# Optimization experiments

Measured on AMD Instinct MI355X. Metric: run time of the kernel, lower is better.

Reference implementation:

```python
import jax, jax.numpy as jnp
import numpy as np

B, D, S, K, A = 4096, 256, 32, 8192, 256
BETA = 0.25  # vq_commitment_beta


def _ln(x, g, b):
    m = jnp.mean(x, axis=-1, keepdims=True)
    v = jnp.var(x, axis=-1, keepdims=True)
    return (x - m) * jax.lax.rsqrt(v + 1e-5) * g + b


def _clin(zr, zi, Wr, Wi, br, bi):
    # torch ComplexLinear: real = Wr(zr) - Wi(zi); imag = Wi(zr) + Wr(zi)
    return (zr @ Wr.T + br) - (zi @ Wi.T + bi), (zr @ Wi.T + bi) + (zi @ Wr.T + br)


def _forward(x_t_r, x_t_i, gw_r, gw_i, mem_r, mem_i, input_gate, vq_emb,
             vis_pal, aud_pal, mem_gate_W, mem_gate_b, mem_addr_W, mem_addr_b,
             mn_gr, mn_br, mn_gi, mn_bi,
             gq_Wr, gq_Wi, gq_br, gq_bi, gk_Wr, gk_Wi, gk_br, gk_bi,
             gv_Wr, gv_Wi, gv_br, gv_bi, sp_Wr, sp_Wi, sp_br, sp_bi,
             cr_Wr, cr_Wi, cr_br, cr_bi):
    # input gate blend (forward_step preamble)
    alpha = jax.nn.sigmoid(input_gate)
    gr = alpha * gw_r + (1.0 - alpha) * x_t_r
    gi = alpha * gw_i + (1.0 - alpha) * x_t_i
    z_flat = jnp.concatenate([gr, gi], -1)  # [B, 2D]

    # ---- EMA_VQ (eval path): cdist + argmin + straight-through ----
    d2 = (jnp.sum(z_flat ** 2, 1, keepdims=True) + jnp.sum(vq_emb ** 2, 1)
          - 2.0 * (z_flat @ vq_emb.T))  # [B, K]
    idx = jnp.argmin(d2, -1)
    z_q = vq_emb[idx]
    vq_loss = BETA * jnp.mean((jax.lax.stop_gradient(z_q) - z_flat) ** 2, -1)
    v_out = z_flat + jax.lax.stop_gradient(z_q - z_flat)
    probs = jnp.mean(jax.nn.one_hot(idx, K, dtype=jnp.float32), 0)
    batch_ent = -jnp.sum(probs * jnp.log(probs + 1e-10)) / jnp.log(jnp.asarray(K, jnp.float32))

    # ---- HermitianGating ----
    qr, qi = _clin(gr, gi, gq_Wr, gq_Wi, gq_br, gq_bi)
    kr, ki = _clin(gr, gi, gk_Wr, gk_Wi, gk_br, gk_bi)
    vr, vi = _clin(gr, gi, gv_Wr, gv_Wi, gv_br, gv_bi)
    gate = jax.nn.sigmoid(jnp.sum(qr * kr + qi * ki, -1, keepdims=True))  # Re(q k*)
    g_out = jnp.concatenate([vr * gate, vi * gate], -1)

    # ---- AssociativeMemory: content read + gated soft-scatter write ----
    sim = jnp.einsum('bsd,bd->bs', mem_r, gr) + jnp.einsum('bsd,bd->bs', mem_i, gi)  # Re(mem* q)
    attn = jax.nn.softmax(sim, -1)
    read_r = jnp.einsum('bs,bsd->bd', attn, mem_r)
    read_i = jnp.einsum('bs,bsd->bd', attn, mem_i)
    m_out = jnp.concatenate([read_r, read_i], -1)
    wgate = jax.nn.sigmoid(z_flat @ mem_gate_W.T + mem_gate_b)  # [B,1]
    ww = jax.nn.softmax(z_flat @ mem_addr_W.T + mem_addr_b, -1)  # [B,S]
    slot_ent = jnp.mean(-jnp.sum(ww * jnp.log(ww + 1e-10), -1))
    eff = wgate[:, :, None] * ww[:, :, None]  # [B,S,1]
    nm_r = _ln((1.0 - eff) * mem_r + eff * gr[:, None, :], mn_gr, mn_br)
    nm_i = _ln((1.0 - eff) * mem_i + eff * gi[:, None, :], mn_gi, mn_bi)

    # ---- HebbianSensory palette attention ----
    sr, si = _clin(gr, gi, sp_Wr, sp_Wi, sp_br, sp_bi)
    zf2 = jnp.concatenate([sr, si], -1)
    vis_attn = jax.nn.softmax(zf2 @ vis_pal.T, -1)
    aud_attn = jax.nn.softmax(zf2 @ aud_pal.T, -1)
    vis = vis_attn @ vis_pal
    aud = aud_attn @ aud_pal
    # experience = vis_c + i*aud_c
    s_out = jnp.concatenate([vis[:, :D] - aud[:, D:], vis[:, D:] + aud[:, :D]], -1)

    # ---- Critic: i * ComplexLinear(z) ----
    c_r, c_i = _clin(gr, gi, cr_Wr, cr_Wi, cr_br, cr_bi)
    c_out = jnp.concatenate([-c_i, c_r], -1)

    out_main = jnp.stack([v_out, g_out, m_out, s_out, c_out], 1)  # [B,5,2D]
    return out_main, nm_r, nm_i, idx, vq_loss, batch_ent, slot_ent


def setup_inputs():
    key = jax.random.key(0)
    ks = iter(jax.random.split(key, 48))
    n = lambda shape, s=1.0: jax.random.normal(next(ks), shape, dtype=jnp.float32) * s
    inp = {
        'x_t_r': n((B, D)), 'x_t_i': n((B, D)),
        'gw_r': n((B, D)), 'gw_i': n((B, D)),
        'mem_r': n((B, S, D)), 'mem_i': n((B, S, D)),
        'input_gate': jnp.zeros((), jnp.float32),
        'vq_emb': jax.random.uniform(next(ks), (K, 2 * D), jnp.float32, -1.0 / np.sqrt(D), 1.0 / np.sqrt(D)),
        'vis_pal': n((A, 2 * D)), 'aud_pal': n((A, 2 * D)),
        'mem_gate_W': n((1, 2 * D), 0.02), 'mem_gate_b': jnp.zeros((1,), jnp.float32),
        'mem_addr_W': n((S, 2 * D), 0.02), 'mem_addr_b': jnp.zeros((S,), jnp.float32),
        'mn_gr': jnp.ones((D,), jnp.float32), 'mn_br': jnp.zeros((D,), jnp.float32),
        'mn_gi': jnp.ones((D,), jnp.float32), 'mn_bi': jnp.zeros((D,), jnp.float32),
    }
    for p in ('gq', 'gk', 'gv', 'sp', 'cr'):
        inp[p + '_Wr'] = n((D, D), 0.05)
        inp[p + '_Wi'] = n((D, D), 0.05)
        inp[p + '_br'] = jnp.zeros((D,), jnp.float32)
        inp[p + '_bi'] = jnp.zeros((D,), jnp.float32)
    return inp


def reference(x_t_r, x_t_i, gw_r, gw_i, mem_r, mem_i, input_gate, vq_emb,
              vis_pal, aud_pal, mem_gate_W, mem_gate_b, mem_addr_W, mem_addr_b,
              mn_gr, mn_br, mn_gi, mn_bi,
              gq_Wr, gq_Wi, gq_br, gq_bi, gk_Wr, gk_Wi, gk_br, gk_bi,
              gv_Wr, gv_Wi, gv_br, gv_bi, sp_Wr, sp_Wi, sp_br, sp_bi,
              cr_Wr, cr_Wi, cr_br, cr_bi):
    return _forward(x_t_r, x_t_i, gw_r, gw_i, mem_r, mem_i, input_gate, vq_emb,
                    vis_pal, aud_pal, mem_gate_W, mem_gate_b, mem_addr_W, mem_addr_b,
                    mn_gr, mn_br, mn_gi, mn_bi,
                    gq_Wr, gq_Wi, gq_br, gq_bi, gk_Wr, gk_Wi, gk_br, gk_bi,
                    gv_Wr, gv_Wi, gv_br, gv_bi, sp_Wr, sp_Wi, sp_br, sp_bi,
                    cr_Wr, cr_Wi, cr_br, cr_bi)
```

## Files before the change

kernel.cpp:

```cpp
#include <hip/hip_runtime.h>
#include <hip/hip_bf16.h>
#include <math.h>

#define BN 4096
#define DN 256
#define SN 32
#define KN 8192
#define AN 256
#define TWO_D 512

typedef unsigned short ushort;
using bf16x8 = __attribute__((ext_vector_type(8))) short;
using f32x4  = __attribute__((ext_vector_type(4))) float;

#define OUT_MAIN 0ull
#define OUT_NMR  10485760ull
#define OUT_NMI  44040192ull
#define OUT_IDX  77594624ull
#define OUT_VQL  77598720ull
#define OUT_BENT 77602816ull
#define OUT_SENT 77602817ull

#define MBYTE (1024ull*1024ull)
#define WS_GR    (0ull)
#define WS_GI    (4ull*MBYTE)
#define WS_Z2H   (8ull*MBYTE)
#define WS_Z2L   (12ull*MBYTE)
#define WS_EH    (16ull*MBYTE)
#define WS_EL    (24ull*MBYTE)
#define WS_E2    (32ull*MBYTE)
#define WS_WBIG  (33ull*MBYTE)
#define WS_BIAS  (36ull*MBYTE)
#define WS_PALC  (37ull*MBYTE)
#define WS_VIST  (38ull*MBYTE)
#define WS_AUDT  (39ull*MBYTE)
#define WS_PVAL  (40ull*MBYTE)
#define WS_PIDX  (42ull*MBYTE)
#define WS_HIST  (44ull*MBYTE)
#define WS_SENT  (44ull*MBYTE + 64ull*1024ull)
#define WS_CL    (45ull*MBYTE)
#define WS_LOGIT (65ull*MBYTE)
#define WS_ATTN  (73ull*MBYTE)
#define WS_VIS   (77ull*MBYTE)
#define WS_AUD   (85ull*MBYTE)

#define DEVINL __device__ __forceinline__

DEVINL ushort f2bf(float f) {
    union { float f; unsigned u; } v; v.f = f;
    unsigned r = v.u + 0x7fffu + ((v.u >> 16) & 1u);
    return (ushort)(r >> 16);
}
DEVINL float bf2f(ushort h) {
    union { unsigned u; float f; } v; v.u = ((unsigned)h) << 16;
    return v.f;
}
DEVINL float sigmoidf_(float x) { return 1.f / (1.f + __expf(-x)); }

__global__ __launch_bounds__(256) void k_prep_vq(const float* __restrict__ emb,
                                                 ushort* __restrict__ eh,
                                                 ushort* __restrict__ el,
                                                 float* __restrict__ e2) {
    int t = threadIdx.x, w = t >> 6, lane = t & 63;
    int row = blockIdx.x * 4 + w;
    const float* er = emb + (size_t)row * 512;
    float acc = 0.f;
    #pragma unroll
    for (int j = 0; j < 8; j++) {
        int k = lane + 64 * j;
        float e = er[k];
        ushort h = f2bf(e);
        eh[(size_t)row * 512 + k] = h;
        el[(size_t)row * 512 + k] = f2bf(e - bf2f(h));
        acc += e * e;
    }
    for (int m = 1; m < 64; m <<= 1) acc += __shfl_xor(acc, m, 64);
    if (lane == 0) e2[row] = acc;
}

__global__ void k_prep_wbig(const float* __restrict__ Wr, const float* __restrict__ Wi,
                            const float* __restrict__ br, const float* __restrict__ bi,
                            ushort* __restrict__ Wb, float* __restrict__ bias) {
    int idx = blockIdx.x * 256 + threadIdx.x;
    int j = idx >> 9, k = idx & 511;
    int part = j >> 8, jj = j & 255;
    float v;
    if (part == 0) v = (k < 256) ? Wr[jj * 256 + k] : -Wi[jj * 256 + (k - 256)];
    else           v = (k < 256) ? Wi[jj * 256 + k] :  Wr[jj * 256 + (k - 256)];
    Wb[idx] = f2bf(v);
    if (k == 0) bias[j] = part ? (br[jj] + bi[jj]) : (br[jj] - bi[jj]);
}

__global__ void k_prep_palcat(const float* __restrict__ vis, const float* __restrict__ aud,
                              ushort* __restrict__ palc) {
    int idx = blockIdx.x * 256 + threadIdx.x;
    int a = idx >> 9, k = idx & 511;
    float v = (a < 256) ? vis[a * 512 + k] : aud[(a - 256) * 512 + k];
    palc[idx] = f2bf(v);
}
__global__ void k_prep_palT(const float* __restrict__ vis, const float* __restrict__ aud,
                            ushort* __restrict__ visT, ushort* __restrict__ audT) {
    int idx = blockIdx.x * 256 + threadIdx.x;
    int j = idx >> 8, a = idx & 255;
    visT[j * 256 + a] = f2bf(vis[a * 512 + j]);
    audT[j * 256 + a] = f2bf(aud[a * 512 + j]);
}

__global__ void k_gate(const float* __restrict__ xr, const float* __restrict__ xi,
                       const float* __restrict__ gwr, const float* __restrict__ gwi,
                       const float* __restrict__ ig,
                       float* __restrict__ gr, float* __restrict__ gi,
                       ushort* __restrict__ z2h, ushort* __restrict__ z2l) {
    int i = blockIdx.x * 256 + threadIdx.x;
    float a = sigmoidf_(ig[0]);
    float r  = a * gwr[i] + (1.f - a) * xr[i];
    float im = a * gwi[i] + (1.f - a) * xi[i];
    gr[i] = r; gi[i] = im;
    int b = i >> 8, d = i & 255;
    size_t z = (size_t)b * 512;
    ushort rh = f2bf(r);  z2h[z + d] = rh;       z2l[z + d] = f2bf(r - bf2f(rh));
    ushort ih = f2bf(im); z2h[z + 256 + d] = ih; z2l[z + 256 + d] = f2bf(im - bf2f(ih));
}

__global__ __launch_bounds__(256) void k_vq_gemm(
    const ushort* __restrict__ Zh, const ushort* __restrict__ Zl,
    const ushort* __restrict__ Eh, const ushort* __restrict__ El,
    const float* __restrict__ e2, float* __restrict__ pval, int* __restrict__ pidx) {
    __shared__ ushort Ah[128 * 40], Al[128 * 40], Bh[128 * 40], Bl[128 * 40];
    const int m0 = blockIdx.y * 128, n0 = blockIdx.x * 128;
    const int t = threadIdx.x;
    const int w = t >> 6, lane = t & 63, q = lane >> 4, ln = lane & 15;
    const int wm = w >> 1, wn = w & 1;
    f32x4 acc[4][4] = {};
    const int lrow = t >> 2, lcol = (t & 3) * 8;
    for (int k0 = 0; k0 < 512; k0 += 32) {
        __syncthreads();
        #pragma unroll
        for (int rep = 0; rep < 2; rep++) {
            int r = lrow + rep * 64;
            *(uint4*)(&Ah[r * 40 + lcol]) = *(const uint4*)(Zh + (size_t)(m0 + r) * 512 + k0 + lcol);
            *(uint4*)(&Al[r * 40 + lcol]) = *(const uint4*)(Zl + (size_t)(m0 + r) * 512 + k0 + lcol);
            *(uint4*)(&Bh[r * 40 + lcol]) = *(const uint4*)(Eh + (size_t)(n0 + r) * 512 + k0 + lcol);
            *(uint4*)(&Bl[r * 40 + lcol]) = *(const uint4*)(El + (size_t)(n0 + r) * 512 + k0 + lcol);
        }
        __syncthreads();
        bf16x8 ah[4], al[4], bh[4], bl[4];
        #pragma unroll
        for (int i = 0; i < 4; i++) {
            int ar = wm * 64 + i * 16 + ln;
            ah[i] = *(const bf16x8*)(&Ah[ar * 40 + q * 8]);
            al[i] = *(const bf16x8*)(&Al[ar * 40 + q * 8]);
            int br = wn * 64 + i * 16 + ln;
            bh[i] = *(const bf16x8*)(&Bh[br * 40 + q * 8]);
            bl[i] = *(const bf16x8*)(&Bl[br * 40 + q * 8]);
        }
        #pragma unroll
        for (int i = 0; i < 4; i++)
            #pragma unroll
            for (int j = 0; j < 4; j++) {
                acc[i][j] = __builtin_amdgcn_mfma_f32_16x16x32_bf16(ah[i], bh[j], acc[i][j], 0, 0, 0);
                acc[i][j] = __builtin_amdgcn_mfma_f32_16x16x32_bf16(ah[i], bl[j], acc[i][j], 0, 0, 0);
                acc[i][j] = __builtin_amdgcn_mfma_f32_16x16x32_bf16(al[i], bh[j], acc[i][j], 0, 0, 0);
            }
    }
    float e2v[4]; int cidx[4];
    #pragma unroll
    for (int j = 0; j < 4; j++) { cidx[j] = n0 + wn * 64 + j * 16 + ln; e2v[j] = e2[cidx[j]]; }
    #pragma unroll
    for (int i = 0; i < 4; i++) {
        #pragma unroll
        for (int reg = 0; reg < 4; reg++) {
            float bv = 3.4e38f; int bc = 0x7fffffff;
            #pragma unroll
            for (int j = 0; j < 4; j++) {
                float s = e2v[j] - 2.f * acc[i][j][reg];
                if (s < bv || (s == bv && cidx[j] < bc)) { bv = s; bc = cidx[j]; }
            }
            for (int m = 1; m < 16; m <<= 1) {
                float ov = __shfl_xor(bv, m, 64);
                int   oc = __shfl_xor(bc, m, 64);
                if (ov < bv || (ov == bv && oc < bc)) { bv = ov; bc = oc; }
            }
            if (ln == 0) {
                int r = m0 + wm * 64 + i * 16 + q * 4 + reg;
                int slot = blockIdx.x * 2 + wn;
                pval[(size_t)r * 128 + slot] = bv;
                pidx[(size_t)r * 128 + slot] = bc;
            }
        }
    }
}

__global__ __launch_bounds__(256) void k_vqfin(
    const float* __restrict__ pval, const int* __restrict__ pidx,
    const float* __restrict__ emb, const float* __restrict__ gr,
    const float* __restrict__ gi, float* __restrict__ out, int* __restrict__ hist) {
    __shared__ float sz[512];
    __shared__ float sv[128];
    __shared__ int   scd[128];
    __shared__ int   topc[8];
    __shared__ double tsc[8];
    __shared__ int   sbc;
    int b = blockIdx.x, t = threadIdx.x;
    sz[t]       = gr[(size_t)b * 256 + t];
    sz[256 + t] = gi[(size_t)b * 256 + t];
    if (t < 128) { sv[t] = pval[(size_t)b * 128 + t]; scd[t] = pidx[(size_t)b * 128 + t]; }
    __syncthreads();
    if (t == 0) {
        for (int j = 0; j < 8; j++) {
            float bv = 3.4e38f; int bi = 0;
            for (int m = 0; m < 128; m++) {
                float v = sv[m];
                if (v < bv || (v == bv && scd[m] < scd[bi])) { bv = v; bi = m; }
            }
            topc[j] = scd[bi];
            sv[bi] = 3.4e38f;
        }
    }
    __syncthreads();
    int w = t >> 6, lane = t & 63;
    for (int rep = 0; rep < 2; rep++) {
        int j = w + rep * 4;
        int c = topc[j];
        const float* e = emb + (size_t)c * 512;
        double acc = 0.0;
        #pragma unroll
        for (int u = 0; u < 8; u++) {
            int k2 = lane + u * 64;
            double d = (double)sz[k2] - (double)e[k2];
            acc += d * d;
        }
        for (int m = 1; m < 64; m <<= 1) acc += __shfl_xor(acc, m, 64);
        if (lane == 0) tsc[j] = acc;
    }
    __syncthreads();
    if (t == 0) {
        double bv = tsc[0]; int bc = topc[0];
        for (int j = 1; j < 8; j++)
            if (tsc[j] < bv || (tsc[j] == bv && topc[j] < bc)) { bv = tsc[j]; bc = topc[j]; }
        sbc = bc;
        out[OUT_IDX + b] = (float)bc;
        out[OUT_VQL + b] = (float)(0.25 * bv / 512.0);
        atomicAdd(&hist[bc], 1);
    }
    __syncthreads();
    const float* e = emb + (size_t)sbc * 512;
    float* om = out + (size_t)b * 2560;
    om[t]       = e[t];
    om[256 + t] = e[256 + t];
}

__global__ __launch_bounds__(256) void k_gemm(
    const ushort* __restrict__ A, int lda,
    const ushort* __restrict__ Bm, int ldb,
    void* __restrict__ C, int ldc,
    int Kd, const float* __restrict__ bias, int obf) {
    __shared__ ushort As[128 * 40], Bs[128 * 40];
    const int m0 = blockIdx.y * 128, n0 = blockIdx.x * 128;
    const int t = threadIdx.x;
    const int w = t >> 6, lane = t & 63, q = lane >> 4, ln = lane & 15;
    const int wm = w >> 1, wn = w & 1;
    f32x4 acc[4][4] = {};
    const int lrow = t >> 2, lcol = (t & 3) * 8;
    for (int k0 = 0; k0 < Kd; k0 += 32) {
        __syncthreads();
        #pragma unroll
        for (int rep = 0; rep < 2; rep++) {
            int r = lrow + rep * 64;
            *(uint4*)(&As[r * 40 + lcol]) = *(const uint4*)(A + (size_t)(m0 + r) * lda + k0 + lcol);
            *(uint4*)(&Bs[r * 40 + lcol]) = *(const uint4*)(Bm + (size_t)(n0 + r) * ldb + k0 + lcol);
        }
        __syncthreads();
        bf16x8 af[4], bfr[4];
        #pragma unroll
        for (int i = 0; i < 4; i++) {
            af[i]  = *(const bf16x8*)(&As[(wm * 64 + i * 16 + ln) * 40 + q * 8]);
            bfr[i] = *(const bf16x8*)(&Bs[(wn * 64 + i * 16 + ln) * 40 + q * 8]);
        }
        #pragma unroll
        for (int i = 0; i < 4; i++)
            #pragma unroll
            for (int j = 0; j < 4; j++)
                acc[i][j] = __builtin_amdgcn_mfma_f32_16x16x32_bf16(af[i], bfr[j], acc[i][j], 0, 0, 0);
    }
    #pragma unroll
    for (int i = 0; i < 4; i++) {
        int r = m0 + wm * 64 + i * 16 + q * 4;
        #pragma unroll
        for (int j = 0; j < 4; j++) {
            int c = n0 + wn * 64 + j * 16 + ln;
            float bb = bias ? bias[c] : 0.f;
            #pragma unroll
            for (int reg = 0; reg < 4; reg++) {
                float v = acc[i][j][reg] + bb;
                if (obf) ((ushort*)C)[(size_t)(r + reg) * ldc + c] = f2bf(v);
                else     ((float*)C)[(size_t)(r + reg) * ldc + c] = v;
            }
        }
    }
}

__global__ __launch_bounds__(256) void k_hermit(const ushort* __restrict__ CL,
                                                float* __restrict__ out) {
    int b = blockIdx.x, t = threadIdx.x;
    const ushort* row = CL + (size_t)b * 2560;
    float qr = bf2f(row[t]), qi = bf2f(row[256 + t]);
    float kr = bf2f(row[512 + t]), ki = bf2f(row[768 + t]);
    float part = qr * kr + qi * ki;
    __shared__ float red[4];
    for (int m = 1; m < 64; m <<= 1) part += __shfl_xor(part, m, 64);
    if ((t & 63) == 0) red[t >> 6] = part;
    __syncthreads();
    float gate = sigmoidf_(red[0] + red[1] + red[2] + red[3]);
    float vr = bf2f(row[1024 + t]), vi = bf2f(row[1280 + t]);
    float* om = out + (size_t)b * 2560;
    om[512 + t] = vr * gate; om[512 + 256 + t] = vi * gate;
    float crr = bf2f(row[2048 + t]), cii = bf2f(row[2304 + t]);
    om[4 * 512 + t] = -cii; om[4 * 512 + 256 + t] = crr;
}

__global__ __launch_bounds__(256) void k_smax(const float* __restrict__ L,
                                              ushort* __restrict__ attn) {
    int b = blockIdx.x, t = threadIdx.x;
    __shared__ float sred[8];
    for (int h = 0; h < 2; h++) {
        float x = L[(size_t)b * 512 + h * 256 + t];
        float mx = x;
        for (int m = 1; m < 64; m <<= 1) mx = fmaxf(mx, __shfl_xor(mx, m, 64));
        if ((t & 63) == 0) sred[t >> 6] = mx;
        __syncthreads();
        mx = fmaxf(fmaxf(sred[0], sred[1]), fmaxf(sred[2], sred[3]));
        float e = __expf(x - mx);
        float su = e;
        for (int m = 1; m < 64; m <<= 1) su += __shfl_xor(su, m, 64);
        if ((t & 63) == 0) sred[4 + (t >> 6)] = su;
        __syncthreads();
        su = sred[4] + sred[5] + sred[6] + sred[7];
        attn[(size_t)b * 512 + h * 256 + t] = f2bf(e / su);
        __syncthreads();
    }
}

__global__ void k_sout(const float* __restrict__ vis, const float* __restrict__ aud,
                       float* __restrict__ out) {
    int i = blockIdx.x * 256 + threadIdx.x;
    int b = i >> 8, d = i & 255;
    const float* v = vis + (size_t)b * 512;
    const float* a = aud + (size_t)b * 512;
    float* om = out + (size_t)b * 2560 + 3 * 512;
    om[d]       = v[d] - a[256 + d];
    om[256 + d] = v[256 + d] + a[d];
}

__global__ __launch_bounds__(256) void k_mem(
    const float* __restrict__ mem_r, const float* __restrict__ mem_i,
    const float* __restrict__ gr, const float* __restrict__ gi,
    const float* __restrict__ gateW, const float* __restrict__ gateB,
    const float* __restrict__ addrW, const float* __restrict__ addrB,
    const float* __restrict__ mgr, const float* __restrict__ mbr,
    const float* __restrict__ mgi, const float* __restrict__ mbi,
    float* __restrict__ out, float* __restrict__ sent) {
    __shared__ float sg[512];
    __shared__ float prt[256], prt2[256];
    __shared__ float ssim[32], swwl[32], satt[32], seff[32];
    __shared__ float smn[32], srs[32];
    int b = blockIdx.x, t = threadIdx.x;
    const float* mr = mem_r + (size_t)b * 8192;
    const float* mi = mem_i + (size_t)b * 8192;
    sg[t]       = gr[(size_t)b * 256 + t];
    sg[256 + t] = gi[(size_t)b * 256 + t];
    __syncthreads();

    {
        int s = t >> 3, j0 = (t & 7) * 32;
        float p = 0.f;
        for (int d = j0; d < j0 + 32; d++)
            p += mr[s * 256 + d] * sg[d] + mi[s * 256 + d] * sg[256 + d];
        prt[t] = p;
    }
    __syncthreads();
    if (t < 32) {
        float v = 0.f;
        for (int j = 0; j < 8; j++) v += prt[t * 8 + j];
        ssim[t] = v;
    }
    __syncthreads();
    {
        int s = t >> 3, j0 = (t & 7) * 64;
        const float* Wrow = addrW + s * 512;
        float p = 0.f;
        for (int k = j0; k < j0 + 64; k++) p += sg[k] * Wrow[k];
        prt[t] = p;
    }
    __syncthreads();
    if (t < 32) {
        float v = addrB[t];
        for (int j = 0; j < 8; j++) v += prt[t * 8 + j];
        swwl[t] = v;
    }
    __syncthreads();
    prt[t] = sg[t] * gateW[t] + sg[256 + t] * gateW[256 + t];
    __syncthreads();
    if (t == 0) {
        float acc = gateB[0];
        for (int j = 0; j < 256; j++) acc += prt[j];
        float wg = sigmoidf_(acc);
        float mx = ssim[0];
        for (int s = 1; s < 32; s++) mx = fmaxf(mx, ssim[s]);
        float su = 0.f;
        for (int s = 0; s < 32; s++) su += __expf(ssim[s] - mx);
        for (int s = 0; s < 32; s++) satt[s] = __expf(ssim[s] - mx) / su;
        mx = swwl[0];
        for (int s = 1; s < 32; s++) mx = fmaxf(mx, swwl[s]);
        su = 0.f;
        for (int s = 0; s < 32; s++) su += __expf(swwl[s] - mx);
        float ent = 0.f;
        for (int s = 0; s < 32; s++) {
            float wv = __expf(swwl[s] - mx) / su;
            ent += -wv * __logf(wv + 1e-10f);
            seff[s] = wg * wv;
        }
        atomicAdd(sent, ent * (1.f / 4096.f));
    }
    __syncthreads();
    {
        float rr = 0.f, ri = 0.f;
        for (int s = 0; s < 32; s++) {
            float a = satt[s];
            rr += a * mr[s * 256 + t];
            ri += a * mi[s * 256 + t];
        }
        float* om = out + (size_t)b * 2560 + 1024;
        om[t] = rr; om[256 + t] = ri;
    }
    for (int half = 0; half < 2; half++) {
        const float* mm  = half ? mi  : mr;
        const float* gg  = half ? mgi : mgr;
        const float* bb2 = half ? mbi : mbr;
        size_t base = (half ? OUT_NMI : OUT_NMR) + (size_t)b * 8192;
        __syncthreads();
        {
            int s = t >> 3, j0 = (t & 7) * 32;
            float eff = seff[s];
            float su = 0.f, sq = 0.f;
            for (int d = j0; d < j0 + 32; d++) {
                float x = (1.f - eff) * mm[s * 256 + d] + eff * sg[half * 256 + d];
                su += x; sq += x * x;
            }
            prt[t] = su; prt2[t] = sq;
        }
        __syncthreads();
        if (t < 32) {
            float su = 0.f, sq = 0.f;
            for (int j = 0; j < 8; j++) { su += prt[t * 8 + j]; sq += prt2[t * 8 + j]; }
            float mn = su * (1.f / 256.f);
            float vr = sq * (1.f / 256.f) - mn * mn;
            smn[t] = mn;
            srs[t] = rsqrtf(vr + 1e-5f);
        }
        __syncthreads();
        {
            float gv = gg[t], bv = bb2[t], zz = sg[half * 256 + t];
            for (int s = 0; s < 32; s++) {
                float eff = seff[s];
                float x = (1.f - eff) * mm[s * 256 + t] + eff * zz;
                out[base + (size_t)s * 256 + t] = (x - smn[s]) * srs[s] * gv + bv;
            }
        }
    }
}

__global__ __launch_bounds__(256) void k_scalars(const int* __restrict__ hist,
                                                 const float* __restrict__ sent,
                                                 float* __restrict__ out) {
    int t = threadIdx.x;
    float local = 0.f;
    for (int k = t; k < 8192; k += 256) {
        float p = (float)hist[k] * (1.f / 4096.f);
        local += -p * __logf(p + 1e-10f);
    }
    __shared__ float red[4];
    for (int m = 1; m < 64; m <<= 1) local += __shfl_xor(local, m, 64);
    if ((t & 63) == 0) red[t >> 6] = local;
    __syncthreads();
    if (t == 0) {
        float bent = (red[0] + red[1] + red[2] + red[3]) / logf(8192.f);
        out[OUT_BENT] = bent;
        out[OUT_SENT] = sent[0];
    }
}

extern "C" void kernel_launch(void* const* d_in, const int* in_sizes, int n_in,
                              void* d_out, int out_size, void* d_ws, size_t ws_size,
                              hipStream_t stream) {
    const float* x_t_r = (const float*)d_in[0];
    const float* x_t_i = (const float*)d_in[1];
    const float* gw_r  = (const float*)d_in[2];
    const float* gw_i  = (const float*)d_in[3];
    const float* mem_r = (const float*)d_in[4];
    const float* mem_i = (const float*)d_in[5];
    const float* ig    = (const float*)d_in[6];
    const float* emb   = (const float*)d_in[7];
    const float* visp  = (const float*)d_in[8];
    const float* audp  = (const float*)d_in[9];
    const float* gateW = (const float*)d_in[10];
    const float* gateB = (const float*)d_in[11];
    const float* addrW = (const float*)d_in[12];
    const float* addrB = (const float*)d_in[13];
    const float* mgr   = (const float*)d_in[14];
    const float* mbr   = (const float*)d_in[15];
    const float* mgi   = (const float*)d_in[16];
    const float* mbi   = (const float*)d_in[17];

    char* w = (char*)d_ws;
    float*  gr    = (float*)(w + WS_GR);
    float*  gi    = (float*)(w + WS_GI);
    ushort* z2h   = (ushort*)(w + WS_Z2H);
    ushort* z2l   = (ushort*)(w + WS_Z2L);
    ushort* eh    = (ushort*)(w + WS_EH);
    ushort* el    = (ushort*)(w + WS_EL);
    float*  e2    = (float*)(w + WS_E2);
    ushort* Wbig  = (ushort*)(w + WS_WBIG);
    float*  biasv = (float*)(w + WS_BIAS);
    ushort* palc  = (ushort*)(w + WS_PALC);
    ushort* visT  = (ushort*)(w + WS_VIST);
    ushort* audT  = (ushort*)(w + WS_AUDT);
    float*  pval  = (float*)(w + WS_PVAL);
    int*    pidx  = (int*)(w + WS_PIDX);
    int*    hist  = (int*)(w + WS_HIST);
    float*  sent  = (float*)(w + WS_SENT);
    ushort* CLb   = (ushort*)(w + WS_CL);
    float*  logit = (float*)(w + WS_LOGIT);
    ushort* attn  = (ushort*)(w + WS_ATTN);
    float*  vis   = (float*)(w + WS_VIS);
    float*  aud   = (float*)(w + WS_AUD);
    float*  out   = (float*)d_out;

    hipMemsetAsync(w + WS_HIST, 0, 8192 * sizeof(int), stream);
    hipMemsetAsync(w + WS_SENT, 0, sizeof(float), stream);

    k_prep_vq<<<KN / 4, 256, 0, stream>>>(emb, eh, el, e2);
    for (int p = 0; p < 5; p++) {
        k_prep_wbig<<<1024, 256, 0, stream>>>(
            (const float*)d_in[18 + p * 4], (const float*)d_in[19 + p * 4],
            (const float*)d_in[20 + p * 4], (const float*)d_in[21 + p * 4],
            Wbig + (size_t)p * 512 * 512, biasv + p * 512);
    }
    k_prep_palcat<<<1024, 256, 0, stream>>>(visp, audp, palc);
    k_prep_palT<<<512, 256, 0, stream>>>(visp, audp, visT, audT);

    k_gate<<<BN, 256, 0, stream>>>(x_t_r, x_t_i, gw_r, gw_i, ig, gr, gi, z2h, z2l);

    k_vq_gemm<<<dim3(64, 32), 256, 0, stream>>>(z2h, z2l, eh, el, e2, pval, pidx);
    k_vqfin<<<BN, 256, 0, stream>>>(pval, pidx, emb, gr, gi, out, hist);

    k_gemm<<<dim3(20, 32), 256, 0, stream>>>(z2h, 512, Wbig, 512, CLb, 2560, 512, biasv, 1);
    k_hermit<<<BN, 256, 0, stream>>>(CLb, out);

    k_gemm<<<dim3(4, 32), 256, 0, stream>>>(CLb + 1536, 2560, palc, 512, logit, 512, 512, nullptr, 0);
    k_smax<<<BN, 256, 0, stream>>>(logit, attn);
    k_gemm<<<dim3(4, 32), 256, 0, stream>>>(attn, 512, visT, 256, vis, 512, 256, nullptr, 0);
    k_gemm<<<dim3(4, 32), 256, 0, stream>>>(attn + 256, 512, audT, 256, aud, 512, 256, nullptr, 0);
    k_sout<<<BN, 256, 0, stream>>>(vis, aud, out);

    k_mem<<<BN, 256, 0, stream>>>(mem_r, mem_i, gr, gi, gateW, gateB, addrW, addrB,
                                  mgr, mbr, mgi, mbi, out, sent);

    k_scalars<<<1, 256, 0, stream>>>(hist, sent, out);
}
```

Before: 1.085 ms.

## Rewrite memory kernel to keep slots in registers with shuffle reductions

The associative-memory kernel now loads each thread's 32 real and 32 imaginary memory values into registers once. Those registers are reused for the similarity, the read, and both LayerNorm passes, where the old code read global memory several times with strided per-thread row access. Dot products and LayerNorm statistics use wave shuffle reductions instead of shared-memory partials. The serial single-thread softmax is parallelised across 32 lanes. This cuts repeated global traffic and synchronisation, but raises register pressure (64 floats per thread) under the new launch bound of 4 blocks.

```diff
diff --git a/kernel.cpp b/kernel.cpp
--- a/kernel.cpp
+++ b/kernel.cpp
@@ -352,7 +352,46 @@
     om[256 + d] = v[256 + d] + a[d];
 }
 
-__global__ __launch_bounds__(256) void k_mem(
+DEVINL void ln_half(float (&v)[32], float zz,
+                    const float* __restrict__ gam, const float* __restrict__ bet,
+                    float* __restrict__ obase, int t, int wp, int hs,
+                    float (*redA)[33], float (*redB)[33],
+                    float* __restrict__ smn, float* __restrict__ srs,
+                    const float* __restrict__ seff) {
+    float keepU = 0.f, keepQ = 0.f;
+    #pragma unroll
+    for (int s = 0; s < 32; s++) {
+        float eff = seff[s];
+        float x = v[s] + eff * (zz - v[s]);
+        v[s] = x;
+        float su = x, sq = x * x;
+        #pragma unroll
+        for (int m = 1; m <= 16; m <<= 1) {
+            su += __shfl_xor(su, m, 64);
+            sq += __shfl_xor(sq, m, 64);
+        }
+        if (hs == s) { keepU = su; keepQ = sq; }
+    }
+    redA[wp][hs] = keepU;
+    redB[wp][hs] = keepQ;
+    __syncthreads();
+    if (t < 32) {
+        float su = 0.f, sq = 0.f;
+        #pragma unroll
+        for (int j = 0; j < 8; j++) { su += redA[j][t]; sq += redB[j][t]; }
+        float mn = su * (1.f / 256.f);
+        float va = sq * (1.f / 256.f) - mn * mn;
+        smn[t] = mn; srs[t] = rsqrtf(va + 1e-5f);
+    }
+    __syncthreads();
+    float gv = gam[t], bv = bet[t];
+    #pragma unroll
+    for (int s = 0; s < 32; s++)
+        obase[(size_t)s * 256 + t] = (v[s] - smn[s]) * srs[s] * gv + bv;
+    __syncthreads();
+}
+
+__global__ __launch_bounds__(256, 4) void k_mem(
     const float* __restrict__ mem_r, const float* __restrict__ mem_i,
     const float* __restrict__ gr, const float* __restrict__ gi,
     const float* __restrict__ gateW, const float* __restrict__ gateB,
@@ -360,114 +399,94 @@
     const float* __restrict__ mgr, const float* __restrict__ mbr,
     const float* __restrict__ mgi, const float* __restrict__ mbi,
     float* __restrict__ out, float* __restrict__ sent) {
-    __shared__ float sg[512];
-    __shared__ float prt[256], prt2[256];
-    __shared__ float ssim[32], swwl[32], satt[32], seff[32];
-    __shared__ float smn[32], srs[32];
-    int b = blockIdx.x, t = threadIdx.x;
+    __shared__ float redA[8][33];
+    __shared__ float redB[8][33];
+    __shared__ float redG[8];
+    __shared__ float satt[32], seff[32], smn[32], srs[32];
+    const int b = blockIdx.x, t = threadIdx.x;
+    const int w = t >> 6, lane = t & 63;
+    const int wp = (w << 1) | (lane >> 5);
+    const int hs = lane & 31;
     const float* mr = mem_r + (size_t)b * 8192;
     const float* mi = mem_i + (size_t)b * 8192;
-    sg[t]       = gr[(size_t)b * 256 + t];
-    sg[256 + t] = gi[(size_t)b * 256 + t];
-    __syncthreads();
+    const float zr = gr[(size_t)b * 256 + t];
+    const float zi = gi[(size_t)b * 256 + t];
+
+    float vr_[32], vi_[32];
+    #pragma unroll
+    for (int s = 0; s < 32; s++) vr_[s] = mr[s * 256 + t];
+    #pragma unroll
+    for (int s = 0; s < 32; s++) vi_[s] = mi[s * 256 + t];
 
     {
-        int s = t >> 3, j0 = (t & 7) * 32;
-        float p = 0.f;
-        for (int d = j0; d < j0 + 32; d++)
-            p += mr[s * 256 + d] * sg[d] + mi[s * 256 + d] * sg[256 + d];
-        prt[t] = p;
-    }
-    __syncthreads();
+        float keepS = 0.f;
+        #pragma unroll
+        for (int s = 0; s < 32; s++) {
+            float ps = vr_[s] * zr + vi_[s] * zi;
+            #pragma unroll
+            for (int m = 1; m <= 16; m <<= 1) ps += __shfl_xor(ps, m, 64);
+            if (hs == s) keepS = ps;
+        }
+        redA[wp][hs] = keepS;
+    }
+    {
+        float keepW = 0.f;
+        #pragma unroll 4
+        for (int s = 0; s < 32; s++) {
+            float pw = addrW[s * 512 + t] * zr + addrW[s * 512 + 256 + t] * zi;
+            #pragma unroll
+            for (int m = 1; m <= 16; m <<= 1) pw += __shfl_xor(pw, m, 64);
+            if (hs == s) keepW = pw;
+        }
+        redB[wp][hs] = keepW;
+    }
+    {
+        float pg = gateW[t] * zr + gateW[256 + t] * zi;
+        #pragma unroll
+        for (int m = 1; m <= 16; m <<= 1) pg += __shfl_xor(pg, m, 64);
+        if (hs == 0) redG[wp] = pg;
+    }
+    __syncthreads();
+
     if (t < 32) {
-        float v = 0.f;
-        for (int j = 0; j < 8; j++) v += prt[t * 8 + j];
-        ssim[t] = v;
-    }
-    __syncthreads();
-    {
-        int s = t >> 3, j0 = (t & 7) * 64;
-        const float* Wrow = addrW + s * 512;
-        float p = 0.f;
-        for (int k = j0; k < j0 + 64; k++) p += sg[k] * Wrow[k];
-        prt[t] = p;
-    }
-    __syncthreads();
-    if (t < 32) {
-        float v = addrB[t];
-        for (int j = 0; j < 8; j++) v += prt[t * 8 + j];
-        swwl[t] = v;
-    }
-    __syncthreads();
-    prt[t] = sg[t] * gateW[t] + sg[256 + t] * gateW[256 + t];
-    __syncthreads();
-    if (t == 0) {
-        float acc = gateB[0];
-        for (int j = 0; j < 256; j++) acc += prt[j];
-        float wg = sigmoidf_(acc);
-        float mx = ssim[0];
-        for (int s = 1; s < 32; s++) mx = fmaxf(mx, ssim[s]);
-        float su = 0.f;
-        for (int s = 0; s < 32; s++) su += __expf(ssim[s] - mx);
-        for (int s = 0; s < 32; s++) satt[s] = __expf(ssim[s] - mx) / su;
-        mx = swwl[0];
-        for (int s = 1; s < 32; s++) mx = fmaxf(mx, swwl[s]);
-        su = 0.f;
-        for (int s = 0; s < 32; s++) su += __expf(swwl[s] - mx);
-        float ent = 0.f;
-        for (int s = 0; s < 32; s++) {
-            float wv = __expf(swwl[s] - mx) / su;
-            ent += -wv * __logf(wv + 1e-10f);
-            seff[s] = wg * wv;
-        }
-        atomicAdd(sent, ent * (1.f / 4096.f));
-    }
-    __syncthreads();
+        float sim = 0.f, wwl = addrB[t], g = gateB[0];
+        #pragma unroll
+        for (int j = 0; j < 8; j++) { sim += redA[j][t]; wwl += redB[j][t]; g += redG[j]; }
+        float wg = sigmoidf_(g);
+        float mx = sim;
+        #pragma unroll
+        for (int m = 1; m <= 16; m <<= 1) mx = fmaxf(mx, __shfl_xor(mx, m, 64));
+        float e = __expf(sim - mx), su = e;
+        #pragma unroll
+        for (int m = 1; m <= 16; m <<= 1) su += __shfl_xor(su, m, 64);
+        satt[t] = e / su;
+        mx = wwl;
+        #pragma unroll
+        for (int m = 1; m <= 16; m <<= 1) mx = fmaxf(mx, __shfl_xor(mx, m, 64));
+        e = __expf(wwl - mx); su = e;
+        #pragma unroll
+        for (int m = 1; m <= 16; m <<= 1) su += __shfl_xor(su, m, 64);
+        float wv = e / su;
+        seff[t] = wg * wv;
+        float ent = -wv * __logf(wv + 1e-10f);
+        #pragma unroll
+        for (int m = 1; m <= 16; m <<= 1) ent += __shfl_xor(ent, m, 64);
+        if (t == 0) atomicAdd(sent, ent * (1.f / 4096.f));
+    }
+    __syncthreads();
+
     {
         float rr = 0.f, ri = 0.f;
-        for (int s = 0; s < 32; s++) {
-            float a = satt[s];
-            rr += a * mr[s * 256 + t];
-            ri += a * mi[s * 256 + t];
-        }
+        #pragma unroll
+        for (int s = 0; s < 32; s++) { float a = satt[s]; rr += a * vr_[s]; ri += a * vi_[s]; }
         float* om = out + (size_t)b * 2560 + 1024;
         om[t] = rr; om[256 + t] = ri;
     }
-    for (int half = 0; half < 2; half++) {
-        const float* mm  = half ? mi  : mr;
-        const float* gg  = half ? mgi : mgr;
-        const float* bb2 = half ? mbi : mbr;
-        size_t base = (half ? OUT_NMI : OUT_NMR) + (size_t)b * 8192;
-        __syncthreads();
-        {
-            int s = t >> 3, j0 = (t & 7) * 32;
-            float eff = seff[s];
-            float su = 0.f, sq = 0.f;
-            for (int d = j0; d < j0 + 32; d++) {
-                float x = (1.f - eff) * mm[s * 256 + d] + eff * sg[half * 256 + d];
-                su += x; sq += x * x;
-            }
-            prt[t] = su; prt2[t] = sq;
-        }
-        __syncthreads();
-        if (t < 32) {
-            float su = 0.f, sq = 0.f;
-            for (int j = 0; j < 8; j++) { su += prt[t * 8 + j]; sq += prt2[t * 8 + j]; }
-            float mn = su * (1.f / 256.f);
-            float vr = sq * (1.f / 256.f) - mn * mn;
-            smn[t] = mn;
-            srs[t] = rsqrtf(vr + 1e-5f);
-        }
-        __syncthreads();
-        {
-            float gv = gg[t], bv = bb2[t], zz = sg[half * 256 + t];
-            for (int s = 0; s < 32; s++) {
-                float eff = seff[s];
-                float x = (1.f - eff) * mm[s * 256 + t] + eff * zz;
-                out[base + (size_t)s * 256 + t] = (x - smn[s]) * srs[s] * gv + bv;
-            }
-        }
-    }
+
+    ln_half(vr_, zr, mgr, mbr, out + OUT_NMR + (size_t)b * 8192,
+            t, wp, hs, redA, redB, smn, srs, seff);
+    ln_half(vi_, zi, mgi, mbi, out + OUT_NMI + (size_t)b * 8192,
+            t, wp, hs, redA, redB, smn, srs, seff);
 }
 
 __global__ __launch_bounds__(256) void k_scalars(const int* __restrict__ hist,
```

New measurement: 1.079 ms. About the same (-0.5%).
